# Kernel tuning notes

Hardware: AMD Instinct MI355X
Metric: run time of the kernel (lower is better)

The kernel has to match this reference:

```python
import jax, jax.numpy as jnp
import numpy as np

BATCH = 4096
M = 50        # CEM candidates per state
N_TOP = 32    # elites
ITERS = 100   # sequential CEM iterations
HIDDEN = 100


def setup_inputs() -> dict:
    key = jax.random.key(0)
    ks = jax.random.split(key, 7)
    states = jax.random.normal(ks[0], (BATCH, 2), dtype=jnp.float32)
    W1 = jax.random.normal(ks[1], (3, HIDDEN), dtype=jnp.float32) * 0.1
    b1 = jnp.zeros((HIDDEN,), dtype=jnp.float32)
    W2 = jax.random.normal(ks[2], (HIDDEN, HIDDEN), dtype=jnp.float32) * 0.1
    b2 = jnp.zeros((HIDDEN,), dtype=jnp.float32)
    W3 = jax.random.normal(ks[3], (HIDDEN, 1), dtype=jnp.float32) * 0.1
    b3 = jnp.zeros((1,), dtype=jnp.float32)
    return {"states": states, "W1": W1, "b1": b1, "W2": W2, "b2": b2, "W3": W3, "b3": b3}


def reference(states, W1, b1, W2, b2, W3, b3):
    batch = states.shape[0]
    states_bm = jnp.broadcast_to(states[:, None, :], (batch, M, 2))

    def qnet(angles):  # angles: (batch, M) -> q: (batch, M)
        x = jnp.concatenate([states_bm, angles[..., None]], axis=-1)  # (batch, M, 3)
        h = jax.nn.relu(x @ W1 + b1)
        h = jax.nn.relu(h @ W2 + b2)
        return (h @ W3 + b3)[..., 0]

    key = jax.random.key(42)
    k0, kloop = jax.random.split(key)
    # iteration 0: uniform random angles in [0, 1)
    angles0 = jax.random.uniform(k0, (batch, M), dtype=jnp.float32)
    q0 = qnet(angles0)

    def step(q, k):
        # NOTE: faithful to source — elites/mu/std are over Q-VALUES, and
        # new "angles" are sampled from Normal(mu_q, std_q).
        top = jax.lax.top_k(q, N_TOP)[0]                 # (batch, N_TOP)
        mu = top.mean(-1)                                # (batch,)
        std = top.std(-1, ddof=1)                        # torch unbiased std
        eps = jax.random.normal(k, (batch, M), dtype=jnp.float32)
        angles = mu[:, None] + std[:, None] * eps        # reparameterized normal
        return qnet(angles), mu

    keys = jax.random.split(kloop, ITERS - 1)
    _, mus = jax.lax.scan(step, q0, keys)
    return mus[-1] * (2.0 * jnp.pi)
```

## Files before the change

kernel.cpp:

```cpp
#include <hip/hip_runtime.h>
#include <math.h>
#include <stdint.h>

#define BATCH 4096
#define MCAND 50
#define NTOP 32
#define HID 100
#define TFL 20200
#define EPS_ROWS 98
#define EPS_ROWSZ (BATCH*MCAND)
#define WS_NEED   (1024u + (size_t)EPS_ROWS*EPS_ROWSZ*4u)

#define MINVC  (-0x1.fffffep-1f)
#define SQRT2C (0x1.6a09e6p+0f)

__device__ __forceinline__ uint32_t rotl32(uint32_t v, int d){ return (v<<d)|(v>>(32-d)); }

__device__ __forceinline__ void tf2x32(uint32_t k0, uint32_t k1, uint32_t x0, uint32_t x1,
                                       uint32_t &o0, uint32_t &o1){
  uint32_t k2 = k0 ^ k1 ^ 0x1BD11BDAu;
  x0 += k0; x1 += k1;
#define RND(r) { x0 += x1; x1 = rotl32(x1,(r)); x1 ^= x0; }
  RND(13) RND(15) RND(26) RND(6)
  x0 += k1; x1 += k2 + 1u;
  RND(17) RND(29) RND(16) RND(24)
  x0 += k2; x1 += k0 + 2u;
  RND(13) RND(15) RND(26) RND(6)
  x0 += k0; x1 += k1 + 3u;
  RND(17) RND(29) RND(16) RND(24)
  x0 += k1; x1 += k2 + 4u;
  RND(13) RND(15) RND(26) RND(6)
  x0 += k2; x1 += k0 + 5u;
#undef RND
  o0 = x0; o1 = x1;
}

__device__ __forceinline__ float erfinv32(float x){
  float w = -log1pf(-x*x);
  float p;
  if (w < 5.0f){
    w = w - 2.5f;
    p = 2.81022636e-08f;
    p = fmaf(p, w, 3.43273939e-07f);
    p = fmaf(p, w, -3.5233877e-06f);
    p = fmaf(p, w, -4.39150654e-06f);
    p = fmaf(p, w, 0.00021858087f);
    p = fmaf(p, w, -0.00125372503f);
    p = fmaf(p, w, -0.00417768164f);
    p = fmaf(p, w, 0.246640727f);
    p = fmaf(p, w, 1.50140941f);
  } else {
    w = sqrtf(w) - 3.0f;
    p = -0.000200214257f;
    p = fmaf(p, w, 0.000100950558f);
    p = fmaf(p, w, 0.00134934322f);
    p = fmaf(p, w, -0.00367342844f);
    p = fmaf(p, w, 0.00573950773f);
    p = fmaf(p, w, -0.0076224613f);
    p = fmaf(p, w, 0.00943887047f);
    p = fmaf(p, w, 1.00167406f);
    p = fmaf(p, w, 2.83297682f);
  }
  return p*x;
}

#define DPPF(v, CTRL) __int_as_float(__builtin_amdgcn_update_dpp( \
    0, __float_as_int(v), (CTRL), 0xF, 0xF, true))
#define DPPI(v, CTRL) __builtin_amdgcn_update_dpp(0, (v), (CTRL), 0xF, 0xF, true)
#define DPPADD(v, CTRL) ((v) + DPPF((v), (CTRL)))

__device__ __forceinline__ float fswap4(float v){
  float a = DPPF(v, 0x114);
  float b = DPPF(v, 0x104);
  return (threadIdx.x & 4) ? a : b;
}
__device__ __forceinline__ int iswap4(int v){
  int a = DPPI(v, 0x114), b = DPPI(v, 0x104);
  return (threadIdx.x & 4) ? a : b;
}
__device__ __forceinline__ float fswap8(float v){
  return DPPF(v, 0x128);
}
__device__ __forceinline__ float fswap16(float v){
#if __has_builtin(__builtin_amdgcn_permlane16_swap)
  auto r = __builtin_amdgcn_permlane16_swap(__float_as_uint(v), __float_as_uint(v), false, false);
  return __uint_as_float((threadIdx.x & 16) ? r[0] : r[1]);
#else
  return __shfl_xor(v, 16, 64);
#endif
}
__device__ __forceinline__ float fswap32(float v){
#if __has_builtin(__builtin_amdgcn_permlane32_swap)
  auto r = __builtin_amdgcn_permlane32_swap(__float_as_uint(v), __float_as_uint(v), false, false);
  return __uint_as_float((threadIdx.x & 32) ? r[0] : r[1]);
#else
  return __shfl_xor(v, 32, 64);
#endif
}

__global__ void keys_kernel(uint32_t* __restrict__ K){
  int tid = threadIdx.x;
  if (tid < 99){
    uint32_t A0, B0, A1, B1;
    tf2x32(0u,42u,0u,2u,A0,A1);
    tf2x32(0u,42u,1u,3u,B0,B1);
    (void)A0; (void)B0;
    uint32_t o0,o1;
    tf2x32(A1,B1,(uint32_t)tid,(uint32_t)(99+tid),o0,o1);
    K[tid]    = o0;
    K[99+tid] = o1;
  }
}

__device__ __forceinline__ float bits2norm(uint32_t bits){
  float fl = __uint_as_float((bits>>9) | 0x3f800000u) - 1.0f;
  float u  = fmaxf(MINVC, fl*2.0f + MINVC);
  return SQRT2C * erfinv32(u);
}

__global__ __launch_bounds__(256) void eps_kernel(const uint32_t* __restrict__ K,
                                                  float* __restrict__ E){
  int id = blockIdx.x*256 + threadIdx.x;
  int t  = id / 102400;
  int g  = id - t*102400;
  uint32_t kk0 = K[2*t], kk1 = K[2*t+1];
  uint32_t r0, r1;
  tf2x32(kk0,kk1,(uint32_t)g,(uint32_t)g+102400u,r0,r1);
  E[(size_t)t*EPS_ROWSZ + g]           = bits2norm(r0);
  E[(size_t)t*EPS_ROWSZ + g + 102400]  = bits2norm(r1);
}

template<bool EPSG>
__global__ __launch_bounds__(512) void cem_kernel(
    const float* __restrict__ states, const float* __restrict__ W1,
    const float* __restrict__ b1,     const float* __restrict__ W2,
    const float* __restrict__ b2,     const float* __restrict__ W3,
    const float* __restrict__ b3,     const float* __restrict__ epsg,
    float* __restrict__ out)
{
  __shared__ __align__(16) float smem[20350];
  float*  const Tb   = smem;
  float2* const T2D  = (float2*)Tb;
  int*    const ORD  = (int*)(Tb + 300);
  float*  const STm  = Tb + 400;
  float*  const AQ   = smem + 20200;
  float*  const EPB  = smem + 20250;

  const int tid  = threadIdx.x;
  const int b    = blockIdx.x;
  const int wv   = tid >> 6;
  const int lane = tid & 63;
  const int gc   = tid >> 3;
  const int gj   = tid & 7;
  const bool gact = (tid < 8*MCAND);

  float w3r[13];
#pragma unroll
  for (int i = 0; i < 13; ++i){
    int n = gj + (i<<3);
    w3r[i] = (n < HID) ? W3[n] : 0.0f;
  }
  const float sB3v = b3[0];

  uint32_t A1k = 0u, B1k = 0u, kk0 = 0u, kk1 = 0u;

  if (tid < HID){
    float u = fmaf(states[2*b], W1[tid], fmaf(states[2*b+1], W1[HID+tid], b1[tid]));
    float v = W1[2*HID+tid];
    float tt = (v != 0.0f) ? (-u / v) : INFINITY;
    Tb[tid]     = u;
    Tb[HID+tid] = v;
    Tb[200+tid] = tt;
  }
  if (tid >= 128 && tid < 128 + MCAND){
    int c = tid - 128;
    uint32_t A0, B0, a1t, b1t;
    tf2x32(0u,42u,0u,2u,A0,a1t);
    tf2x32(0u,42u,1u,3u,B0,b1t);
    uint32_t gidx = (uint32_t)b*MCAND + (uint32_t)c;
    uint32_t r0,r1,bits;
    if (gidx < 102400u){ tf2x32(A0,B0,gidx,gidx+102400u,r0,r1); bits = r0; }
    else               { tf2x32(A0,B0,gidx-102400u,gidx,r0,r1); bits = r1; }
    AQ[c] = __uint_as_float((bits>>9) | 0x3f800000u) - 1.0f;
  }
  if (!EPSG && wv == 7){
    uint32_t A0, B0;
    tf2x32(0u,42u,0u,2u,A0,A1k);
    tf2x32(0u,42u,1u,3u,B0,B1k);
    { uint32_t i0 = 0u; uint32_t x,y; tf2x32(A1k,B1k, i0, 99u+i0, x, y); kk0 = x; }
    { uint32_t i1 = 1u; uint32_t x,y; tf2x32(A1k,B1k, i1, 99u+i1, x, y); kk1 = x; }
  }
  __syncthreads();

  if (tid < HID){
    float tk = Tb[200+tid];
    int rk = 0;
    for (int j2 = 0; j2 < HID; ++j2){
      float tj = Tb[200+j2];
      rk += (tj < tk || (tj == tk && j2 < tid)) ? 1 : 0;
    }
    float u = Tb[tid], v = Tb[HID+tid];
    int neg = (v < 0.0f || (v == 0.0f && u > 0.0f)) ? 1 : 0;
    STm[rk] = tk;
    ORD[rk] = tid | (neg << 7);
  }
  __syncthreads();

  int kpA = 0, kpB = 0; float cuA = 0.f, cvA = 0.f, cuB = 0.f, cvB = 0.f;
  if (wv == 0){
    kpA = ORD[lane];
    int kiA = kpA & 127;
    float uA = Tb[kiA], vA = Tb[HID+kiA];
    cuA = (kpA & 128) ? -uA : uA;
    cvA = (kpA & 128) ? -vA : vA;
    if (lane < 36){
      kpB = ORD[64+lane];
      int kiB = kpB & 127;
      float uB = Tb[kiB], vB = Tb[HID+kiB];
      cuB = (kpB & 128) ? -uB : uB;
      cvB = (kpB & 128) ? -vB : vB;
    }
  }
  float st_r[13];
#pragma unroll
  for (int i = 0; i < 13; ++i){
    int idx = gj*13 + i;
    st_r[i] = (idx < HID) ? STm[idx] : INFINITY;
  }
  __syncthreads();

  if (wv == 0){
    const int L = lane;
    float a10 = b2[L], a20 = 0.0f;
    float a11 = (L < 36) ? b2[64+L] : 0.0f, a21 = 0.0f;
#pragma unroll 8
    for (int rr = 0; rr < 64; ++rr){
      int   kp = __builtin_amdgcn_readlane(kpA, rr);
      float cu = __int_as_float(__builtin_amdgcn_readlane(__float_as_int(cuA), rr));
      float cv = __int_as_float(__builtin_amdgcn_readlane(__float_as_int(cvA), rr));
      int k = kp & 127;
      float bu = (kp & 128) ? -cu : 0.0f;
      float bv = (kp & 128) ? -cv : 0.0f;
      float w0 = W2[k*HID + L];
      a10 = fmaf(bu, w0, a10); a20 = fmaf(bv, w0, a20);
      if (L < 36){
        float w1 = W2[k*HID + 64+L];
        a11 = fmaf(bu, w1, a11); a21 = fmaf(bv, w1, a21);
      }
    }
#pragma unroll 6
    for (int rr = 0; rr < 36; ++rr){
      int   kp = __builtin_amdgcn_readlane(kpB, rr);
      float cu = __int_as_float(__builtin_amdgcn_readlane(__float_as_int(cuB), rr));
      float cv = __int_as_float(__builtin_amdgcn_readlane(__float_as_int(cvB), rr));
      int k = kp & 127;
      float bu = (kp & 128) ? -cu : 0.0f;
      float bv = (kp & 128) ? -cv : 0.0f;
      float w0 = W2[k*HID + L];
      a10 = fmaf(bu, w0, a10); a20 = fmaf(bv, w0, a20);
      if (L < 36){
        float w1 = W2[k*HID + 64+L];
        a11 = fmaf(bu, w1, a11); a21 = fmaf(bv, w1, a21);
      }
    }
    { float2 f; f.x = a10; f.y = a20; T2D[L] = f; }
    if (L < 36){ float2 f; f.x = a11; f.y = a21; T2D[64+L] = f; }
#pragma unroll 8
    for (int rr = 0; rr < 64; ++rr){
      int   kp = __builtin_amdgcn_readlane(kpA, rr);
      float cu = __int_as_float(__builtin_amdgcn_readlane(__float_as_int(cuA), rr));
      float cv = __int_as_float(__builtin_amdgcn_readlane(__float_as_int(cvA), rr));
      int k = kp & 127;
      float w0 = W2[k*HID + L];
      a10 = fmaf(cu, w0, a10); a20 = fmaf(cv, w0, a20);
      { float2 f; f.x = a10; f.y = a20; T2D[(rr+1)*HID + L] = f; }
      if (L < 36){
        float w1 = W2[k*HID + 64+L];
        a11 = fmaf(cu, w1, a11); a21 = fmaf(cv, w1, a21);
        float2 f; f.x = a11; f.y = a21; T2D[(rr+1)*HID + 64+L] = f;
      }
    }
#pragma unroll 6
    for (int rr = 0; rr < 36; ++rr){
      int   kp = __builtin_amdgcn_readlane(kpB, rr);
      float cu = __int_as_float(__builtin_amdgcn_readlane(__float_as_int(cuB), rr));
      float cv = __int_as_float(__builtin_amdgcn_readlane(__float_as_int(cvB), rr));
      int k = kp & 127;
      float w0 = W2[k*HID + L];
      a10 = fmaf(cu, w0, a10); a20 = fmaf(cv, w0, a20);
      { float2 f; f.x = a10; f.y = a20; T2D[(65+rr)*HID + L] = f; }
      if (L < 36){
        float w1 = W2[k*HID + 64+L];
        a11 = fmaf(cu, w1, a11); a21 = fmaf(cv, w1, a21);
        float2 f; f.x = a11; f.y = a21; T2D[(65+rr)*HID + 64+L] = f;
      }
    }
  }

  float pref = 0.0f;
  if (EPSG && wv == 7 && lane < MCAND){
    const float* Eb = epsg + (size_t)b*MCAND + (size_t)lane;
    EPB[lane] = Eb[0];
    pref = Eb[(size_t)1*EPS_ROWSZ];
  }
  __syncthreads();

#pragma unroll 1
  for (int t = 0; t < 99; ++t){
    if (gact){
      const float av = AQ[gc];
      int rk = 0;
#pragma unroll
      for (int i = 0; i < 13; ++i) rk += (st_r[i] < av) ? 1 : 0;
      rk += DPPI(rk, 0xB1);
      rk += DPPI(rk, 0x4E);
      rk += iswap4(rk);
      const char* rowp = (const char*)T2D + (((rk*HID) + gj) << 3);
      float acc = 0.0f;
#pragma unroll
      for (int i = 0; i < 12; ++i){
        float2 tv = *(const float2*)(rowp + (i << 6));
        float h = fmaxf(fmaf(av, tv.y, tv.x), 0.0f);
        acc = fmaf(h, w3r[i], acc);
      }
      if (gj < 4){
        float2 tv = *(const float2*)(rowp + (12 << 6));
        float h = fmaxf(fmaf(av, tv.y, tv.x), 0.0f);
        acc = fmaf(h, w3r[12], acc);
      }
      acc = DPPADD(acc, 0xB1);
      acc = DPPADD(acc, 0x4E);
      acc += fswap4(acc);
      if (gj == 0) AQ[gc] = acc;
    }
    if (EPSG){
      if (wv == 7 && lane < MCAND && (t+1) < EPS_ROWS){
        EPB[((t+1)&1)*MCAND + lane] = pref;
        if ((t+2) < EPS_ROWS)
          pref = epsg[(size_t)(t+2)*EPS_ROWSZ + (size_t)b*MCAND + (size_t)lane];
      }
    } else if (wv == 7 && t < EPS_ROWS && lane < MCAND){
      uint32_t gidx = (uint32_t)b*MCAND + (uint32_t)lane;
      uint32_t r0, r1, bits;
      if (gidx < 102400u){ tf2x32(kk0,kk1,gidx,gidx+102400u,r0,r1); bits = r0; }
      else               { tf2x32(kk0,kk1,gidx-102400u,gidx,r0,r1); bits = r1; }
      EPB[lane] = bits2norm(bits);
    }
    __syncthreads();

    if (wv == 0){
      float q = (lane < MCAND) ? (AQ[lane] + sB3v) : -INFINITY;
      float v = q;
#define BST(KK, JJ, PV) { float pv = (PV); bool lower = (lane & (JJ)) == 0; \
        bool asc = (lane & (KK)) != 0; float mn = fminf(v, pv), mx = fmaxf(v, pv); \
        v = (lower == asc) ? mn : mx; }
      BST(2, 1,  DPPF(v, 0xB1))
      BST(4, 2,  DPPF(v, 0x4E))
      BST(4, 1,  DPPF(v, 0xB1))
      BST(8, 4,  fswap4(v))
      BST(8, 2,  DPPF(v, 0x4E))
      BST(8, 1,  DPPF(v, 0xB1))
      BST(16, 8, fswap8(v))
      BST(16, 4, fswap4(v))
      BST(16, 2, DPPF(v, 0x4E))
      BST(16, 1, DPPF(v, 0xB1))
      BST(32, 16, fswap16(v))
      BST(32, 8,  fswap8(v))
      BST(32, 4,  fswap4(v))
      BST(32, 2,  DPPF(v, 0x4E))
      BST(32, 1,  DPPF(v, 0xB1))
#undef BST
      {
        float pv = fswap32(v);
        v = ((lane & 32) == 0) ? fmaxf(v, pv) : fminf(v, pv);
      }
      float sv = (lane < NTOP) ? v : 0.0f;
      sv += fswap32(sv);
      sv += fswap16(sv);
      sv += fswap8(sv);
      sv += fswap4(sv);
      sv = DPPADD(sv, 0x4E);
      sv = DPPADD(sv, 0xB1);
      float mun = sv / 32.0f;
      float dv = (lane < NTOP) ? (v - mun) : 0.0f;
      float s2 = dv*dv;
      s2 += fswap32(s2);
      s2 += fswap16(s2);
      s2 += fswap8(s2);
      s2 += fswap4(s2);
      s2 = DPPADD(s2, 0x4E);
      s2 = DPPADD(s2, 0xB1);
      float stdv = sqrtf(s2 / 31.0f);
      if (t == 98){
        if (lane == 0) out[b] = mun * 6.2831854820251465f;
      } else if (lane < MCAND){
        float e = EPSG ? EPB[(t&1)*MCAND + lane] : EPB[lane];
        AQ[lane] = fmaf(stdv, e, mun);
      }
    } else if (!EPSG && wv == 7 && t < EPS_ROWS){
      uint32_t nt = (uint32_t)(t + 1);
      { uint32_t i0 = 2u*nt;      uint32_t ii = (i0 < 99u) ? i0 : (i0 - 99u);
        uint32_t x,y; tf2x32(A1k,B1k, ii, 99u+ii, x, y); kk0 = (i0 < 99u) ? x : y; }
      { uint32_t i1 = 2u*nt + 1u; uint32_t ii = (i1 < 99u) ? i1 : (i1 - 99u);
        uint32_t x,y; tf2x32(A1k,B1k, ii, 99u+ii, x, y); kk1 = (i1 < 99u) ? x : y; }
    }
    __syncthreads();
  }
}

extern "C" void kernel_launch(void* const* d_in, const int* in_sizes, int n_in,
                              void* d_out, int out_size, void* d_ws, size_t ws_size,
                              hipStream_t stream) {
  const float* states = (const float*)d_in[0];
  const float* W1     = (const float*)d_in[1];
  const float* b1     = (const float*)d_in[2];
  const float* W2     = (const float*)d_in[3];
  const float* b2     = (const float*)d_in[4];
  const float* W3     = (const float*)d_in[5];
  const float* b3     = (const float*)d_in[6];
  float* out = (float*)d_out;

  if (d_ws != nullptr && ws_size >= WS_NEED){
    uint32_t* K = (uint32_t*)d_ws;
    float*    E = (float*)((char*)d_ws + 1024);
    hipLaunchKernelGGL(keys_kernel, dim3(1), dim3(128), 0, stream, K);
    hipLaunchKernelGGL(eps_kernel, dim3(EPS_ROWS*102400/256), dim3(256), 0, stream, K, E);
    hipLaunchKernelGGL(HIP_KERNEL_NAME(cem_kernel<true>), dim3(BATCH), dim3(512), 0, stream,
                       states, W1, b1, W2, b2, W3, b3, (const float*)E, out);
  } else {
    hipLaunchKernelGGL(HIP_KERNEL_NAME(cem_kernel<false>), dim3(BATCH), dim3(512), 0, stream,
                       states, W1, b1, W2, b2, W3, b3, (const float*)nullptr, out);
  }
}
```

Baseline: 1.313 ms.

## Replace bitonic top-k with per-wave radix select and drop second barrier

```diff
diff --git a/kernel.cpp b/kernel.cpp
--- a/kernel.cpp
+++ b/kernel.cpp
@@ -98,6 +98,20 @@
 #endif
 }
 
+__device__ __forceinline__ float tsum64(float v){
+  v += fswap32(v);
+  v += fswap16(v);
+  v += fswap8(v);
+  v += fswap4(v);
+  v = DPPADD(v, 0x4E);
+  v = DPPADD(v, 0xB1);
+  return v;
+}
+
+__device__ __forceinline__ void bar_lgkm(){
+  asm volatile("s_waitcnt lgkmcnt(0)\n\ts_barrier" ::: "memory");
+}
+
 __global__ void keys_kernel(uint32_t* __restrict__ K){
   int tid = threadIdx.x;
   if (tid < 99){
@@ -138,13 +152,13 @@
     const float* __restrict__ b3,     const float* __restrict__ epsg,
     float* __restrict__ out)
 {
-  __shared__ __align__(16) float smem[20350];
+  __shared__ __align__(16) float smem[20450];
   float*  const Tb   = smem;
   float2* const T2D  = (float2*)Tb;
   int*    const ORD  = (int*)(Tb + 300);
   float*  const STm  = Tb + 400;
-  float*  const AQ   = smem + 20200;
-  float*  const EPB  = smem + 20250;
+  float*  const QB   = smem + 20200;
+  float*  const EPB  = smem + 20300;
 
   const int tid  = threadIdx.x;
   const int b    = blockIdx.x;
@@ -181,7 +195,7 @@
     uint32_t r0,r1,bits;
     if (gidx < 102400u){ tf2x32(A0,B0,gidx,gidx+102400u,r0,r1); bits = r0; }
     else               { tf2x32(A0,B0,gidx-102400u,gidx,r0,r1); bits = r1; }
-    AQ[c] = __uint_as_float((bits>>9) | 0x3f800000u) - 1.0f;
+    QB[50 + c] = __uint_as_float((bits>>9) | 0x3f800000u) - 1.0f;
   }
   if (!EPSG && wv == 7){
     uint32_t A0, B0;
@@ -229,6 +243,7 @@
   }
   __syncthreads();
 
+  float pref = 0.0f;
   if (wv == 0){
     const int L = lane;
     float a10 = b2[L], a20 = 0.0f;
@@ -295,20 +310,21 @@
         float2 f; f.x = a11; f.y = a21; T2D[(65+rr)*HID + 64+L] = f;
       }
     }
-  }
-
-  float pref = 0.0f;
-  if (EPSG && wv == 7 && lane < MCAND){
+  } else if (EPSG && wv == 7 && lane < MCAND){
     const float* Eb = epsg + (size_t)b*MCAND + (size_t)lane;
     EPB[lane] = Eb[0];
     pref = Eb[(size_t)1*EPS_ROWSZ];
   }
   __syncthreads();
 
+  float aregs = 0.0f;
+  if (gact) aregs = QB[50 + gc];
+
 #pragma unroll 1
   for (int t = 0; t < 99; ++t){
+    const int par = t & 1;
     if (gact){
-      const float av = AQ[gc];
+      const float av = aregs;
       int rk = 0;
 #pragma unroll
       for (int i = 0; i < 13; ++i) rk += (st_r[i] < av) ? 1 : 0;
@@ -331,80 +347,59 @@
       acc = DPPADD(acc, 0xB1);
       acc = DPPADD(acc, 0x4E);
       acc += fswap4(acc);
-      if (gj == 0) AQ[gc] = acc;
-    }
-    if (EPSG){
-      if (wv == 7 && lane < MCAND && (t+1) < EPS_ROWS){
-        EPB[((t+1)&1)*MCAND + lane] = pref;
-        if ((t+2) < EPS_ROWS)
-          pref = epsg[(size_t)(t+2)*EPS_ROWSZ + (size_t)b*MCAND + (size_t)lane];
-      }
-    } else if (wv == 7 && t < EPS_ROWS && lane < MCAND){
-      uint32_t gidx = (uint32_t)b*MCAND + (uint32_t)lane;
-      uint32_t r0, r1, bits;
-      if (gidx < 102400u){ tf2x32(kk0,kk1,gidx,gidx+102400u,r0,r1); bits = r0; }
-      else               { tf2x32(kk0,kk1,gidx-102400u,gidx,r0,r1); bits = r1; }
-      EPB[lane] = bits2norm(bits);
-    }
-    __syncthreads();
-
-    if (wv == 0){
-      float q = (lane < MCAND) ? (AQ[lane] + sB3v) : -INFINITY;
-      float v = q;
-#define BST(KK, JJ, PV) { float pv = (PV); bool lower = (lane & (JJ)) == 0; \
-        bool asc = (lane & (KK)) != 0; float mn = fminf(v, pv), mx = fmaxf(v, pv); \
-        v = (lower == asc) ? mn : mx; }
-      BST(2, 1,  DPPF(v, 0xB1))
-      BST(4, 2,  DPPF(v, 0x4E))
-      BST(4, 1,  DPPF(v, 0xB1))
-      BST(8, 4,  fswap4(v))
-      BST(8, 2,  DPPF(v, 0x4E))
-      BST(8, 1,  DPPF(v, 0xB1))
-      BST(16, 8, fswap8(v))
-      BST(16, 4, fswap4(v))
-      BST(16, 2, DPPF(v, 0x4E))
-      BST(16, 1, DPPF(v, 0xB1))
-      BST(32, 16, fswap16(v))
-      BST(32, 8,  fswap8(v))
-      BST(32, 4,  fswap4(v))
-      BST(32, 2,  DPPF(v, 0x4E))
-      BST(32, 1,  DPPF(v, 0xB1))
-#undef BST
-      {
-        float pv = fswap32(v);
-        v = ((lane & 32) == 0) ? fmaxf(v, pv) : fminf(v, pv);
-      }
-      float sv = (lane < NTOP) ? v : 0.0f;
-      sv += fswap32(sv);
-      sv += fswap16(sv);
-      sv += fswap8(sv);
-      sv += fswap4(sv);
-      sv = DPPADD(sv, 0x4E);
-      sv = DPPADD(sv, 0xB1);
-      float mun = sv / 32.0f;
-      float dv = (lane < NTOP) ? (v - mun) : 0.0f;
-      float s2 = dv*dv;
-      s2 += fswap32(s2);
-      s2 += fswap16(s2);
-      s2 += fswap8(s2);
-      s2 += fswap4(s2);
-      s2 = DPPADD(s2, 0x4E);
-      s2 = DPPADD(s2, 0xB1);
+      if (gj == 0) QB[par*MCAND + gc] = acc;
+    } else if (wv == 7 && lane < MCAND){
+      if (EPSG){
+        if ((t+1) < EPS_ROWS){
+          EPB[((t+1)%3)*MCAND + lane] = pref;
+          if ((t+2) < EPS_ROWS)
+            pref = epsg[(size_t)(t+2)*EPS_ROWSZ + (size_t)b*MCAND + (size_t)lane];
+        }
+      } else if (t < EPS_ROWS){
+        uint32_t gidx = (uint32_t)b*MCAND + (uint32_t)lane;
+        uint32_t r0, r1, bits;
+        if (gidx < 102400u){ tf2x32(kk0,kk1,gidx,gidx+102400u,r0,r1); bits = r0; }
+        else               { tf2x32(kk0,kk1,gidx-102400u,gidx,r0,r1); bits = r1; }
+        EPB[(t%3)*MCAND + lane] = bits2norm(bits);
+      }
+    }
+    bar_lgkm();
+
+    if (wv < 7){
+      float qf = (lane < MCAND) ? (QB[par*MCAND + lane] + sB3v) : -INFINITY;
+      uint32_t sbits = __float_as_uint(qf);
+      uint32_t uval  = (sbits & 0x80000000u) ? ~sbits : (sbits | 0x80000000u);
+      uint32_t selu = 0u;
+#pragma unroll
+      for (int bb = 31; bb >= 0; --bb){
+        uint32_t cand = selu | (1u << bb);
+        unsigned long long blt = __ballot(uval >= cand);
+        if (__popcll(blt) >= NTOP) selu = cand;
+      }
+      unsigned long long gmask = __ballot(uval > selu);
+      int cnt_gt = __popcll(gmask);
+      float mth = (float)(NTOP - cnt_gt);
+      uint32_t tb = (selu & 0x80000000u) ? (selu & 0x7FFFFFFFu) : ~selu;
+      float theta = __uint_as_float(tb);
+      bool top = (uval > selu);
+      float sum = tsum64(top ? qf : 0.0f) + mth * theta;
+      float mun = sum / 32.0f;
+      float dvt = theta - mun;
+      float dv  = top ? (qf - mun) : 0.0f;
+      float s2  = tsum64(dv * dv) + mth * dvt * dvt;
       float stdv = sqrtf(s2 / 31.0f);
       if (t == 98){
-        if (lane == 0) out[b] = mun * 6.2831854820251465f;
-      } else if (lane < MCAND){
-        float e = EPSG ? EPB[(t&1)*MCAND + lane] : EPB[lane];
-        AQ[lane] = fmaf(stdv, e, mun);
-      }
-    } else if (!EPSG && wv == 7 && t < EPS_ROWS){
+        if (wv == 0 && lane == 0) out[b] = mun * 6.2831854820251465f;
+      } else if (gact){
+        aregs = fmaf(stdv, EPB[(t%3)*MCAND + gc], mun);
+      }
+    } else if (!EPSG && wv == 7 && t < EPS_ROWS - 1){
       uint32_t nt = (uint32_t)(t + 1);
       { uint32_t i0 = 2u*nt;      uint32_t ii = (i0 < 99u) ? i0 : (i0 - 99u);
         uint32_t x,y; tf2x32(A1k,B1k, ii, 99u+ii, x, y); kk0 = (i0 < 99u) ? x : y; }
       { uint32_t i1 = 2u*nt + 1u; uint32_t ii = (i1 < 99u) ? i1 : (i1 - 99u);
         uint32_t x,y; tf2x32(A1k,B1k, ii, 99u+ii, x, y); kk1 = (i1 < 99u) ? x : y; }
     }
-    __syncthreads();
   }
 }
 
```

Result: slower. 1.950 ms (+48.6%).
